# Kernel tuning notes

Hardware: AMD Instinct MI355X
Metric: run time of the kernel (lower is better)

The kernel has to match this reference:

```python
import jax, jax.numpy as jnp
import numpy as np
import math

DIM = 4096
N_HEADS = 32
N_KV_HEADS = 8
HEAD_DIM = DIM // N_HEADS  # 128
N_REP = N_HEADS // N_KV_HEADS  # 4
BATCH = 1
SEQ = 2048
ROPE_THETA = 10000.0


def setup_inputs() -> dict:
    key = jax.random.key(0)
    ks = jax.random.split(key, 6)
    x = jax.random.normal(ks[0], (BATCH, SEQ, DIM), dtype=jnp.float32)
    # torch nn.Linear weights are [out_features, in_features]
    s = 1.0 / math.sqrt(DIM)
    wq = jax.random.normal(ks[1], (N_HEADS * HEAD_DIM, DIM), dtype=jnp.float32) * s
    wk = jax.random.normal(ks[2], (N_KV_HEADS * HEAD_DIM, DIM), dtype=jnp.float32) * s
    wv = jax.random.normal(ks[3], (N_KV_HEADS * HEAD_DIM, DIM), dtype=jnp.float32) * s
    wo = jax.random.normal(ks[4], (DIM, N_HEADS * HEAD_DIM), dtype=jnp.float32) * s
    # precomputed rotary frequencies (real/imag parts of freqs_cis)
    inv_freq = 1.0 / (ROPE_THETA ** (jnp.arange(0, HEAD_DIM, 2, dtype=jnp.float32) / HEAD_DIM))
    t = jnp.arange(SEQ, dtype=jnp.float32)
    freqs = jnp.outer(t, inv_freq)  # [S, HEAD_DIM//2]
    return {"x": x, "wq": wq, "wk": wk, "wv": wv, "wo": wo,
            "freqs_cos": jnp.cos(freqs), "freqs_sin": jnp.sin(freqs)}


def _apply_rotary(t, cos, sin):
    # t: [B, S, H, HD]; cos/sin: [S, HD//2]
    B, S, H, HD = t.shape
    tr = t.reshape(B, S, H, HD // 2, 2)
    re, im = tr[..., 0], tr[..., 1]
    c = cos[None, :, None, :]
    s = sin[None, :, None, :]
    out_re = re * c - im * s
    out_im = re * s + im * c
    return jnp.stack([out_re, out_im], axis=-1).reshape(B, S, H, HD)


def reference(x, wq, wk, wv, wo, freqs_cos, freqs_sin):
    B, S, _ = x.shape
    q = jnp.einsum('bsd,od->bso', x, wq).reshape(B, S, N_HEADS, HEAD_DIM)
    k = jnp.einsum('bsd,od->bso', x, wk).reshape(B, S, N_KV_HEADS, HEAD_DIM)
    v = jnp.einsum('bsd,od->bso', x, wv).reshape(B, S, N_KV_HEADS, HEAD_DIM)
    q = _apply_rotary(q, freqs_cos, freqs_sin)
    k = _apply_rotary(k, freqs_cos, freqs_sin)
    # repeat kv heads (GQA): [B,S,Hkv,HD] -> [B,S,H,HD]
    k = jnp.repeat(k, N_REP, axis=2)
    v = jnp.repeat(v, N_REP, axis=2)
    # SDPA with causal mask
    scale = 1.0 / math.sqrt(HEAD_DIM)
    scores = jnp.einsum('bqhd,bkhd->bhqk', q, k) * scale
    causal = jnp.tril(jnp.ones((S, S), dtype=bool))
    scores = jnp.where(causal[None, None], scores, jnp.finfo(scores.dtype).min)
    attn = jax.nn.softmax(scores, axis=-1)
    y = jnp.einsum('bhqk,bkhd->bqhd', attn, v).reshape(B, S, N_HEADS * HEAD_DIM)
    return jnp.einsum('bso,do->bsd', y, wo)
```

## Files before the change

kernel.cpp:

```cpp
#include <hip/hip_runtime.h>
#include <hip/hip_bf16.h>
#include <stdint.h>

typedef unsigned short u16;
typedef __bf16 bf16_8 __attribute__((ext_vector_type(8)));
typedef float f32x4 __attribute__((ext_vector_type(4)));

#define SEQ 2048
#define DIM 4096
#define NH 32
#define NKV 8
#define HD 128
#define QSCALE_LOG2E 0.12753785222167917f

__device__ inline u16 f2bf(float f) {
    unsigned int u = __float_as_uint(f);
    unsigned int r = (u + 0x7fffu + ((u >> 16) & 1u)) >> 16;
    return (u16)r;
}

__device__ inline void async16(const void* g, void* l) {
    __builtin_amdgcn_global_load_lds(
        (const __attribute__((address_space(1))) void*)g,
        (__attribute__((address_space(3))) void*)l, 16, 0, 0);
}

__global__ __launch_bounds__(256) void cast_all(const float* __restrict__ x,
                                                const float* __restrict__ wq,
                                                const float* __restrict__ wk,
                                                const float* __restrict__ wv,
                                                const float* __restrict__ wo,
                                                u16* __restrict__ dst) {
    size_t i4 = (size_t)blockIdx.x * 256 + threadIdx.x;
    size_t e = i4 * 4;
    const float* src;
    size_t off;
    if (e < 8388608ull)       { src = x;  off = 0; }
    else if (e < 25165824ull) { src = wq; off = 8388608ull; }
    else if (e < 29360128ull) { src = wk; off = 25165824ull; }
    else if (e < 33554432ull) { src = wv; off = 29360128ull; }
    else                      { src = wo; off = 33554432ull; }
    float4 v = ((const float4*)src)[i4 - off / 4];
    ushort4 o;
    o.x = f2bf(v.x); o.y = f2bf(v.y); o.z = f2bf(v.z); o.w = f2bf(v.w);
    ((ushort4*)dst)[i4] = o;
}

template <int MODE>
__global__ __launch_bounds__(256, 3) void gemm_rs(const u16* __restrict__ A,
                                                  const u16* __restrict__ B,
                                                  void* __restrict__ C0,
                                                  void* __restrict__ C1,
                                                  void* __restrict__ C2,
                                                  const float* __restrict__ fc,
                                                  const float* __restrict__ fs,
                                                  int M, int N, int K) {
    __shared__ u16 As[2 * 128 * 32];
    __shared__ u16 Bs[2 * 128 * 32];

    const int tid = threadIdx.x;
    const int lane = tid & 63;
    const int wid = tid >> 6;
    const int wr = wid >> 1;
    const int wc = wid & 1;
    const int quad = lane >> 4;
    const int l16 = lane & 15;

    const int gx = gridDim.x, gy = gridDim.y;
    int id = blockIdx.y * gx + blockIdx.x;
    const int xcd = id & 7;
    const int j = id >> 3;
    const int hy = gy >> 1;
    const int jm = j % hy;
    const int jn = j / hy;
    const int bm = ((xcd >> 2) * hy + jm) * 128;
    const int bn = ((xcd & 3) * (gx >> 2) + jn) * 128;

    f32x4 acc[4][4] = {};

    const int srow = tid >> 1;
    const int shalf = tid & 1;
    const int s0 = (shalf * 2) ^ ((srow >> 1) & 3);
    const int s1 = (shalf * 2 + 1) ^ ((srow >> 1) & 3);
    const size_t arowK = (size_t)(bm + srow) * K;
    const size_t browK = (size_t)(bn + srow) * K;
    const int cs = quad ^ ((l16 >> 1) & 3);
    const int wm = wr * 64;
    const int wn = wc * 64;

#define GLOAD(t, A0, A1, B0, B1)                                  \
    {                                                             \
        const size_t ko = (size_t)((t) << 5) + shalf * 16;        \
        A0 = *(const uint4*)&A[arowK + ko];                       \
        A1 = *(const uint4*)&A[arowK + ko + 8];                   \
        B0 = *(const uint4*)&B[browK + ko];                       \
        B1 = *(const uint4*)&B[browK + ko + 8];                   \
    }

#define LWRITE(buf, A0, A1, B0, B1)                               \
    {                                                             \
        u16* pa = &As[(buf) * 4096 + srow * 32];                  \
        *(uint4*)&pa[s0 * 8] = A0;                                \
        *(uint4*)&pa[s1 * 8] = A1;                                \
        u16* pb = &Bs[(buf) * 4096 + srow * 32];                  \
        *(uint4*)&pb[s0 * 8] = B0;                                \
        *(uint4*)&pb[s1 * 8] = B1;                                \
    }

#define COMPUTE(buf)                                                           \
    {                                                                          \
        const u16* as = &As[(buf) * 4096];                                     \
        const u16* bs = &Bs[(buf) * 4096];                                     \
        bf16_8 a[4], b[4];                                                     \
        _Pragma("unroll") for (int i = 0; i < 4; ++i)                          \
            a[i] = *(const bf16_8*)&as[(wm + i * 16 + l16) * 32 + cs * 8];     \
        _Pragma("unroll") for (int j2 = 0; j2 < 4; ++j2)                       \
            b[j2] = *(const bf16_8*)&bs[(wn + j2 * 16 + l16) * 32 + cs * 8];   \
        __builtin_amdgcn_s_setprio(1);                                         \
        _Pragma("unroll") for (int i = 0; i < 4; ++i)                          \
        _Pragma("unroll") for (int j2 = 0; j2 < 4; ++j2)                       \
            acc[i][j2] = __builtin_amdgcn_mfma_f32_16x16x32_bf16(a[i], b[j2],  \
                                                                acc[i][j2], 0, 0, 0); \
        __builtin_amdgcn_s_setprio(0);                                         \
    }

#define LGKM_BAR()                                                \
    asm volatile("s_waitcnt lgkmcnt(0)" ::: "memory");            \
    __builtin_amdgcn_s_barrier()

    const int NT = K >> 5;
    uint4 xa0, xa1, xb0, xb1;
    uint4 ya0, ya1, yb0, yb1;

    GLOAD(0, xa0, xa1, xb0, xb1);
    LWRITE(0, xa0, xa1, xb0, xb1);
    GLOAD(1, ya0, ya1, yb0, yb1);
    LGKM_BAR();

    for (int t = 0; t < NT - 2; t += 2) {
        COMPUTE(0);
        GLOAD(t + 2, xa0, xa1, xb0, xb1);
        LWRITE(1, ya0, ya1, yb0, yb1);
        LGKM_BAR();
        COMPUTE(1);
        GLOAD(t + 3, ya0, ya1, yb0, yb1);
        LWRITE(0, xa0, xa1, xb0, xb1);
        LGKM_BAR();
    }
    COMPUTE(0);
    LWRITE(1, ya0, ya1, yb0, yb1);
    LGKM_BAR();
    COMPUTE(1);

#undef GLOAD
#undef LWRITE
#undef COMPUTE
#undef LGKM_BAR

    if (MODE == 0) {
        float* Cf = (float*)C0;
#pragma unroll
        for (int i = 0; i < 4; ++i)
#pragma unroll
            for (int j2 = 0; j2 < 4; ++j2)
#pragma unroll
                for (int r = 0; r < 4; ++r)
                    Cf[(size_t)(bm + wm + i * 16 + quad * 4 + r) * N + (bn + wn + j2 * 16 + l16)] =
                        acc[i][j2][r];
    } else {
        u16* Qb = (u16*)C0;
        u16* Kb = (u16*)C1;
        u16* Vt = (u16*)C2;
        if (bn < 5120) {
            const bool isQ = bn < 4096;
            const float osc = isQ ? QSCALE_LOG2E : 1.0f;
#pragma unroll
            for (int i = 0; i < 4; ++i)
#pragma unroll
                for (int j2 = 0; j2 < 4; ++j2) {
                    int n = bn + wn + j2 * 16 + l16;
                    int pp = (n & 127) >> 1;
                    bool odd = (l16 & 1);
#pragma unroll
                    for (int r = 0; r < 4; ++r) {
                        int m = bm + wm + i * 16 + quad * 4 + r;
                        float v = acc[i][j2][r];
                        float u = __shfl_xor(v, 1);
                        float c = fc[m * 64 + pp];
                        float s = fs[m * 64 + pp];
                        float o = (odd ? (u * s + v * c) : (v * c - u * s)) * osc;
                        if (isQ)
                            Qb[(size_t)m * 4096 + n] = f2bf(o);
                        else
                            Kb[(size_t)m * 1024 + (n - 4096)] = f2bf(o);
                    }
                }
        } else {
#pragma unroll
            for (int i = 0; i < 4; ++i)
#pragma unroll
                for (int j2 = 0; j2 < 4; ++j2) {
                    int n = bn + wn + j2 * 16 + l16;
                    ushort4 o;
                    o.x = f2bf(acc[i][j2][0]);
                    o.y = f2bf(acc[i][j2][1]);
                    o.z = f2bf(acc[i][j2][2]);
                    o.w = f2bf(acc[i][j2][3]);
                    *(ushort4*)&Vt[(size_t)(n - 5120) * SEQ + (bm + wm + i * 16 + quad * 4)] = o;
                }
        }
    }
}

__global__ __launch_bounds__(256, 4) void attn_k(const u16* __restrict__ Q,
                                                 const u16* __restrict__ Kb,
                                                 const u16* __restrict__ Vt,
                                                 u16* __restrict__ Y) {
    __shared__ u16 Ks[64 * 128];
    __shared__ u16 Vs[128 * 64];
    __shared__ u16 Ps[4 * 16 * 64];
    const int tid = threadIdx.x;
    const int lane = tid & 63;
    const int w = tid >> 6;
    const int quad = lane >> 4;
    const int l16 = lane & 15;
    const int id = blockIdx.x;
    const int qt = 31 - (id >> 5);
    const int h = id & 31;
    const int kvh = h >> 2;
    const size_t qrow0 = (size_t)qt * 64;

    bf16_8 qf[4];
#pragma unroll
    for (int ks = 0; ks < 4; ++ks)
        qf[ks] = *(const bf16_8*)&Q[(qrow0 + w * 16 + l16) * DIM + h * HD + ks * 32 + quad * 8];

    f32x4 po[8] = {};
    float lsum = 0.f;

    char* psbase = (char*)Ps + w * 2048 + l16 * 128;
    const int sw = (l16 & 7) << 1;

    for (int kt = 0; kt <= qt; ++kt) {
#pragma unroll
        for (int r = 0; r < 4; ++r) {
            int S = r * 256 + tid;
            {
                int row = S >> 4, slot = S & 15;
                int chunk = slot ^ (row & 15);
                const char* g = (const char*)Kb +
                    (((size_t)kt * 64 + row) * 1024 + kvh * HD + chunk * 8) * 2;
                async16(g, (char*)Ks + S * 16);
            }
            {
                int row = S >> 3, slot = S & 7;
                int chunk = slot ^ (row & 7);
                const char* g = (const char*)Vt +
                    (((size_t)(kvh * HD + row)) * SEQ + kt * 64 + chunk * 8) * 2;
                async16(g, (char*)Vs + S * 16);
            }
        }
        __syncthreads();

        f32x4 sc[4] = {};
#pragma unroll
        for (int ks = 0; ks < 4; ++ks)
#pragma unroll
            for (int jb = 0; jb < 4; ++jb) {
                bf16_8 kb = *(const bf16_8*)&Ks[(jb * 16 + l16) * 128 + ((ks * 4 + quad) ^ l16) * 8];
                sc[jb] = __builtin_amdgcn_mfma_f32_16x16x32_bf16(kb, qf[ks], sc[jb], 0, 0, 0);
            }

        float pv[4][4];
#pragma unroll
        for (int jb = 0; jb < 4; ++jb)
#pragma unroll
            for (int r = 0; r < 4; ++r)
                pv[jb][r] = exp2f(sc[jb][r]);

        if (kt == qt) {
            int qloc = w * 16 + l16;
#pragma unroll
            for (int jb = 0; jb < 4; ++jb)
#pragma unroll
                for (int r = 0; r < 4; ++r)
                    if (jb * 16 + quad * 4 + r > qloc) pv[jb][r] = 0.f;
        }

#pragma unroll
        for (int jb = 0; jb < 4; ++jb) {
            lsum += (pv[jb][0] + pv[jb][1]) + (pv[jb][2] + pv[jb][3]);
            ushort4 pk;
            pk.x = f2bf(pv[jb][0]);
            pk.y = f2bf(pv[jb][1]);
            pk.z = f2bf(pv[jb][2]);
            pk.w = f2bf(pv[jb][3]);
            int c = jb * 4 + quad;
            *(ushort4*)(psbase + ((c ^ sw) << 3)) = pk;
        }

#pragma unroll
        for (int ks = 0; ks < 2; ++ks) {
            int c = ks * 8 + quad * 2;
            bf16_8 pf = *(const bf16_8*)(psbase + ((c ^ sw) << 3));
#pragma unroll
            for (int n = 0; n < 8; ++n) {
                bf16_8 vf = *(const bf16_8*)&Vs[(n * 16 + l16) * 64 + (((ks * 4 + quad) ^ (l16 & 7))) * 8];
                po[n] = __builtin_amdgcn_mfma_f32_16x16x32_bf16(pf, vf, po[n], 0, 0, 0);
            }
        }
        __syncthreads();
    }

    lsum += __shfl_xor(lsum, 16);
    lsum += __shfl_xor(lsum, 32);
    float inv = 1.f / lsum;
#pragma unroll
    for (int r = 0; r < 4; ++r) {
        float invr = __shfl(inv, quad * 4 + r);
        size_t row = qrow0 + w * 16 + quad * 4 + r;
#pragma unroll
        for (int n = 0; n < 8; ++n)
            Y[row * DIM + h * HD + n * 16 + l16] = f2bf(po[n][r] * invr);
    }
}

extern "C" void kernel_launch(void* const* d_in, const int* in_sizes, int n_in,
                              void* d_out, int out_size, void* d_ws, size_t ws_size,
                              hipStream_t stream) {
    const float* x  = (const float*)d_in[0];
    const float* wq = (const float*)d_in[1];
    const float* wk = (const float*)d_in[2];
    const float* wv = (const float*)d_in[3];
    const float* wo = (const float*)d_in[4];
    const float* fc = (const float*)d_in[5];
    const float* fs = (const float*)d_in[6];

    char* ws = (char*)d_ws;
    const size_t MB = 1u << 20;
    u16* xb    = (u16*)(ws);
    u16* wqkvb = (u16*)(ws + 16 * MB);
    u16* wob   = (u16*)(ws + 64 * MB);
    u16* Qb    = (u16*)(ws + 96 * MB);
    u16* Kb    = (u16*)(ws + 112 * MB);
    u16* Vtb   = (u16*)(ws + 116 * MB);
    u16* Yb    = (u16*)(ws + 120 * MB);

    cast_all<<<49152, 256, 0, stream>>>(x, wq, wk, wv, wo, (u16*)ws);

    gemm_rs<1><<<dim3(48, 16), 256, 0, stream>>>(xb, wqkvb, Qb, Kb, Vtb, fc, fs,
                                                 2048, 6144, 4096);

    attn_k<<<dim3(1024), 256, 0, stream>>>(Qb, Kb, Vtb, Yb);

    gemm_rs<0><<<dim3(32, 16), 256, 0, stream>>>(Yb, wob, (float*)d_out, nullptr, nullptr,
                                                 nullptr, nullptr, 2048, 4096, 4096);
}
```

Measured before the change: 506.2 us.

## Replace register-staged double-buffered GEMM with single-buffer direct-to-LDS loads

Rewrites the main loop of both bf16 GEMMs to load tiles straight from global memory into LDS with async global_load_lds. It uses a single shared buffer guarded by two barriers per k-step instead of the previous register-staged double buffering. This removes the staging registers and the LDS write instructions and halves LDS use. The cost is losing the overlap of the next tile's global loads with the current tile's MFMA work. The launch-bounds occupancy hint and the MFMA priority boosts are also dropped.

Result: slower. 520.3 us (+2.8%).

```diff
diff --git a/kernel.cpp b/kernel.cpp
--- a/kernel.cpp
+++ b/kernel.cpp
@@ -47,24 +47,23 @@
 }
 
 template <int MODE>
-__global__ __launch_bounds__(256, 3) void gemm_rs(const u16* __restrict__ A,
-                                                  const u16* __restrict__ B,
-                                                  void* __restrict__ C0,
-                                                  void* __restrict__ C1,
-                                                  void* __restrict__ C2,
-                                                  const float* __restrict__ fc,
-                                                  const float* __restrict__ fs,
-                                                  int M, int N, int K) {
-    __shared__ u16 As[2 * 128 * 32];
-    __shared__ u16 Bs[2 * 128 * 32];
-
+__global__ __launch_bounds__(256) void gemm_bt(const u16* __restrict__ A,
+                                               const u16* __restrict__ B,
+                                               void* __restrict__ C0,
+                                               void* __restrict__ C1,
+                                               void* __restrict__ C2,
+                                               const float* __restrict__ fc,
+                                               const float* __restrict__ fs,
+                                               int M, int N, int K) {
+    __shared__ u16 As[128 * 32];
+    __shared__ u16 Bs[128 * 32];
     const int tid = threadIdx.x;
     const int lane = tid & 63;
     const int wid = tid >> 6;
-    const int wr = wid >> 1;
-    const int wc = wid & 1;
     const int quad = lane >> 4;
     const int l16 = lane & 15;
+    const int wm = (wid >> 1) * 64;
+    const int wn = (wid & 1) * 64;
 
     const int gx = gridDim.x, gy = gridDim.y;
     int id = blockIdx.y * gx + blockIdx.x;
@@ -78,84 +77,34 @@
 
     f32x4 acc[4][4] = {};
 
-    const int srow = tid >> 1;
-    const int shalf = tid & 1;
-    const int s0 = (shalf * 2) ^ ((srow >> 1) & 3);
-    const int s1 = (shalf * 2 + 1) ^ ((srow >> 1) & 3);
-    const size_t arowK = (size_t)(bm + srow) * K;
-    const size_t browK = (size_t)(bn + srow) * K;
-    const int cs = quad ^ ((l16 >> 1) & 3);
-    const int wm = wr * 64;
-    const int wn = wc * 64;
-
-#define GLOAD(t, A0, A1, B0, B1)                                  \
-    {                                                             \
-        const size_t ko = (size_t)((t) << 5) + shalf * 16;        \
-        A0 = *(const uint4*)&A[arowK + ko];                       \
-        A1 = *(const uint4*)&A[arowK + ko + 8];                   \
-        B0 = *(const uint4*)&B[browK + ko];                       \
-        B1 = *(const uint4*)&B[browK + ko + 8];                   \
+    for (int k0 = 0; k0 < K; k0 += 32) {
+#pragma unroll
+        for (int r = 0; r < 2; ++r) {
+            int S = r * 256 + tid;
+            int row = S >> 2;
+            int slot = S & 3;
+            int chunk = slot ^ ((row >> 1) & 3);
+            const char* ga = (const char*)A + ((size_t)(bm + row) * K + k0 + chunk * 8) * 2;
+            async16(ga, (char*)As + S * 16);
+            const char* gb = (const char*)B + ((size_t)(bn + row) * K + k0 + chunk * 8) * 2;
+            async16(gb, (char*)Bs + S * 16);
+        }
+        __syncthreads();
+        const int cs = quad ^ ((l16 >> 1) & 3);
+        bf16_8 a[4], b[4];
+#pragma unroll
+        for (int i = 0; i < 4; ++i)
+            a[i] = *(const bf16_8*)&As[(wm + i * 16 + l16) * 32 + cs * 8];
+#pragma unroll
+        for (int j2 = 0; j2 < 4; ++j2)
+            b[j2] = *(const bf16_8*)&Bs[(wn + j2 * 16 + l16) * 32 + cs * 8];
+#pragma unroll
+        for (int i = 0; i < 4; ++i)
+#pragma unroll
+            for (int j2 = 0; j2 < 4; ++j2)
+                acc[i][j2] = __builtin_amdgcn_mfma_f32_16x16x32_bf16(a[i], b[j2], acc[i][j2], 0, 0, 0);
+        __syncthreads();
     }
-
-#define LWRITE(buf, A0, A1, B0, B1)                               \
-    {                                                             \
-        u16* pa = &As[(buf) * 4096 + srow * 32];                  \
-        *(uint4*)&pa[s0 * 8] = A0;                                \
-        *(uint4*)&pa[s1 * 8] = A1;                                \
-        u16* pb = &Bs[(buf) * 4096 + srow * 32];                  \
-        *(uint4*)&pb[s0 * 8] = B0;                                \
-        *(uint4*)&pb[s1 * 8] = B1;                                \
-    }
-
-#define COMPUTE(buf)                                                           \
-    {                                                                          \
-        const u16* as = &As[(buf) * 4096];                                     \
-        const u16* bs = &Bs[(buf) * 4096];                                     \
-        bf16_8 a[4], b[4];                                                     \
-        _Pragma("unroll") for (int i = 0; i < 4; ++i)                          \
-            a[i] = *(const bf16_8*)&as[(wm + i * 16 + l16) * 32 + cs * 8];     \
-        _Pragma("unroll") for (int j2 = 0; j2 < 4; ++j2)                       \
-            b[j2] = *(const bf16_8*)&bs[(wn + j2 * 16 + l16) * 32 + cs * 8];   \
-        __builtin_amdgcn_s_setprio(1);                                         \
-        _Pragma("unroll") for (int i = 0; i < 4; ++i)                          \
-        _Pragma("unroll") for (int j2 = 0; j2 < 4; ++j2)                       \
-            acc[i][j2] = __builtin_amdgcn_mfma_f32_16x16x32_bf16(a[i], b[j2],  \
-                                                                acc[i][j2], 0, 0, 0); \
-        __builtin_amdgcn_s_setprio(0);                                         \
-    }
-
-#define LGKM_BAR()                                                \
-    asm volatile("s_waitcnt lgkmcnt(0)" ::: "memory");            \
-    __builtin_amdgcn_s_barrier()
-
-    const int NT = K >> 5;
-    uint4 xa0, xa1, xb0, xb1;
-    uint4 ya0, ya1, yb0, yb1;
-
-    GLOAD(0, xa0, xa1, xb0, xb1);
-    LWRITE(0, xa0, xa1, xb0, xb1);
-    GLOAD(1, ya0, ya1, yb0, yb1);
-    LGKM_BAR();
-
-    for (int t = 0; t < NT - 2; t += 2) {
-        COMPUTE(0);
-        GLOAD(t + 2, xa0, xa1, xb0, xb1);
-        LWRITE(1, ya0, ya1, yb0, yb1);
-        LGKM_BAR();
-        COMPUTE(1);
-        GLOAD(t + 3, ya0, ya1, yb0, yb1);
-        LWRITE(0, xa0, xa1, xb0, xb1);
-        LGKM_BAR();
-    }
-    COMPUTE(0);
-    LWRITE(1, ya0, ya1, yb0, yb1);
-    LGKM_BAR();
-    COMPUTE(1);
-
-#undef GLOAD
-#undef LWRITE
-#undef COMPUTE
-#undef LGKM_BAR
 
     if (MODE == 0) {
         float* Cf = (float*)C0;
@@ -348,11 +297,11 @@
 
     cast_all<<<49152, 256, 0, stream>>>(x, wq, wk, wv, wo, (u16*)ws);
 
-    gemm_rs<1><<<dim3(48, 16), 256, 0, stream>>>(xb, wqkvb, Qb, Kb, Vtb, fc, fs,
+    gemm_bt<1><<<dim3(48, 16), 256, 0, stream>>>(xb, wqkvb, Qb, Kb, Vtb, fc, fs,
                                                  2048, 6144, 4096);
 
     attn_k<<<dim3(1024), 256, 0, stream>>>(Qb, Kb, Vtb, Yb);
 
-    gemm_rs<0><<<dim3(32, 16), 256, 0, stream>>>(Yb, wob, (float*)d_out, nullptr, nullptr,
+    gemm_bt<0><<<dim3(32, 16), 256, 0, stream>>>(Yb, wob, (float*)d_out, nullptr, nullptr,
                                                  nullptr, nullptr, 2048, 4096, 4096);
 }
```
